# Kernel tuning notes

Measured on AMD Instinct MI355X. Metric: run time of the kernel, lower is better.

Reference implementation:

```python
import jax, jax.numpy as jnp
import numpy as np

N, E, D_IN, D_HID, D_OUT = 50000, 800000, 128, 128, 64

def setup_inputs() -> dict:
    key = jax.random.key(0)
    ks = jax.random.split(key, 20)
    inp = {
        'x': jax.random.normal(ks[0], (N, D_IN), dtype=jnp.float32),
        'edge_index': jax.random.randint(ks[1], (2, E), 0, N, dtype=jnp.int64),
        'edge_attr': jax.random.normal(ks[2], (E, 16), dtype=jnp.float32),
        'edge_weight': jax.random.uniform(ks[3], (E,), dtype=jnp.float32),
    }
    dims = [(D_IN, D_HID), (D_HID, D_HID), (D_HID, D_OUT)]
    for i, (di, do) in enumerate(dims):
        s = 1.0 / np.sqrt(di)
        inp[f'Wl{i}'] = jax.random.uniform(ks[4 + 5 * i], (di, do), minval=-s, maxval=s, dtype=jnp.float32)
        inp[f'bl{i}'] = jnp.zeros((do,), dtype=jnp.float32)
        inp[f'Wr{i}'] = jax.random.uniform(ks[5 + 5 * i], (di, do), minval=-s, maxval=s, dtype=jnp.float32)
        inp[f'Ws{i}'] = jax.random.uniform(ks[6 + 5 * i], (di, do), minval=-s, maxval=s, dtype=jnp.float32)
        inp[f'bs{i}'] = jnp.zeros((do,), dtype=jnp.float32)
    return inp


def _sage(x, src, dst, Wl, bl, Wr):
    # mean aggregation of source features at target nodes (PyG SAGEConv)
    msg = x[src]                                               # [E, d] gather
    ssum = jax.ops.segment_sum(msg, dst, num_segments=N)        # [N, d]
    cnt = jax.ops.segment_sum(jnp.ones((src.shape[0],), x.dtype), dst, num_segments=N)
    agg = ssum / jnp.maximum(cnt, 1.0)[:, None]
    return agg @ Wl + bl + x @ Wr                               # lin_l(agg) + lin_r(x)


def reference(x, edge_index, edge_attr, edge_weight,
              Wl0, bl0, Wr0, Ws0, bs0,
              Wl1, bl1, Wr1, Ws1, bs1,
              Wl2, bl2, Wr2, Ws2, bs2):
    src, dst = edge_index[0], edge_index[1]
    h = jax.nn.relu(_sage(x, src, dst, Wl0, bl0, Wr0) + x @ Ws0 + bs0)
    h = jax.nn.relu(_sage(h, src, dst, Wl1, bl1, Wr1) + h @ Ws1 + bs1)
    out = _sage(h, src, dst, Wl2, bl2, Wr2) + h @ Ws2 + bs2
    return out
```

## Files before the change

### kernel.cpp

```cpp
#include <hip/hip_runtime.h>
#include <hip/hip_bf16.h>


#define LB __launch_bounds__

typedef __attribute__((ext_vector_type(8))) short short8;
typedef __attribute__((ext_vector_type(4))) float f32x4;

__device__ __forceinline__ unsigned short bf16_rne(float f) {
  unsigned u = __builtin_bit_cast(unsigned, f);
  unsigned r = u + 0x7fffu + ((u >> 16) & 1u);
  return (unsigned short)(r >> 16);
}
__device__ __forceinline__ float bf16_to_f(unsigned short us) {
  return __builtin_bit_cast(float, (unsigned)us << 16);
}
__device__ __forceinline__ float bits_to_f(unsigned u) {
  return __builtin_bit_cast(float, u);
}

__device__ __forceinline__ void async16(const void* g, void* l) {
  __builtin_amdgcn_global_load_lds((const __attribute__((address_space(1))) unsigned*)g,
                                   (__attribute__((address_space(3))) unsigned*)l, 16, 0, 0);
}

#define BCAP 8192
#define P1_CHUNK 4096

__device__ __forceinline__ void p1_body(int bid, const int* __restrict__ src,
                                        const int* __restrict__ dst, int* __restrict__ bcnt,
                                        int2* __restrict__ pairs, int E) {
  __shared__ int cnt[256];
  __shared__ int base[256];
  const int tid = threadIdx.x;
  cnt[tid] = 0;
  __syncthreads();
  const int e0 = bid * P1_CHUNK;
  int myb[16], myr[16], mys[16], myd[16];
#pragma unroll
  for (int i = 0; i < 16; ++i) {
    int e = e0 + i * 256 + tid;
    myb[i] = -1;
    if (e < E) {
      int s = src[e], d = dst[e];
      int b = d >> 8;
      myb[i] = b;
      mys[i] = s;
      myd[i] = d;
      myr[i] = atomicAdd(&cnt[b], 1);
    }
  }
  __syncthreads();
  base[tid] = (cnt[tid] > 0) ? atomicAdd(&bcnt[tid], cnt[tid]) : 0;
  __syncthreads();
#pragma unroll
  for (int i = 0; i < 16; ++i) {
    int b = myb[i];
    if (b >= 0) {
      int p = base[b] + myr[i];
      if (p < BCAP) pairs[(size_t)b * BCAP + p] = make_int2(mys[i], myd[i]);
    }
  }
}

__device__ __forceinline__ void p234_body(int b, const int2* __restrict__ pairs,
                                          const int* __restrict__ bcnt, int* __restrict__ gcounter,
                                          int* __restrict__ row_start, int* __restrict__ deg_arr,
                                          float* __restrict__ scale, int* __restrict__ srcs, int N) {
  __shared__ int h[256];
  __shared__ int sc[256];
  __shared__ int cur[256];
  __shared__ int shared_bb;
  const int tid = threadIdx.x;
  h[tid] = 0;
  __syncthreads();
  int m = bcnt[b];
  if (m > BCAP) m = BCAP;
  for (int i = tid; i < m; i += 256) {
    atomicAdd(&h[pairs[(size_t)b * BCAP + i].y & 255], 1);
  }
  __syncthreads();
  const int deg = h[tid];
  sc[tid] = deg;
  __syncthreads();
  for (int off = 1; off < 256; off <<= 1) {
    int add = (tid >= off) ? sc[tid - off] : 0;
    __syncthreads();
    sc[tid] += add;
    __syncthreads();
  }
  if (tid == 0) shared_bb = atomicAdd(gcounter, sc[255]);
  __syncthreads();
  const int abs_off = shared_bb + sc[tid] - deg;
  const int node = b * 256 + tid;
  if (node < N) {
    row_start[node] = abs_off;
    deg_arr[node] = deg;
    scale[node] = 1.0f / (float)(deg > 1 ? deg : 1);
  }
  cur[tid] = abs_off;
  __syncthreads();
  for (int i = tid; i < m; i += 256) {
    int2 pr = pairs[(size_t)b * BCAP + i];
    int p = atomicAdd(&cur[pr.y & 255], 1);
    srcs[p] = pr.x;
  }
}

__device__ __forceinline__ void wpack_body(int wb, const float* __restrict__ Wl0,
                                           const float* __restrict__ Wr0,
                                           const float* __restrict__ Ws0,
                                           const float* __restrict__ bl0,
                                           const float* __restrict__ bs0,
                                           const float* __restrict__ Wl1,
                                           const float* __restrict__ Wr1,
                                           const float* __restrict__ Ws1,
                                           const float* __restrict__ bl1,
                                           const float* __restrict__ bs1,
                                           const float* __restrict__ Wl2,
                                           const float* __restrict__ Wr2,
                                           const float* __restrict__ Ws2,
                                           const float* __restrict__ bl2,
                                           const float* __restrict__ bs2, ushort* __restrict__ Bh0,
                                           ushort* __restrict__ Bo0, float* __restrict__ bb0,
                                           ushort* __restrict__ Bh1, ushort* __restrict__ Bo1,
                                           float* __restrict__ bb1, ushort* __restrict__ Bh2,
                                           ushort* __restrict__ Bo2, float* __restrict__ bb2) {
  const int layer = wb >> 7;
  const int xb = wb & 127;
  const float *Wl, *Wr, *Ws, *bl, *bs;
  ushort *Bh, *Bo;
  float* bb;
  int M;
  if (layer == 0) {
    Wl = Wl0; Wr = Wr0; Ws = Ws0; bl = bl0; bs = bs0; Bh = Bh0; Bo = Bo0; bb = bb0; M = 256;
  } else if (layer == 1) {
    Wl = Wl1; Wr = Wr1; Ws = Ws1; bl = bl1; bs = bs1; Bh = Bh1; Bo = Bo1; bb = bb1; M = 256;
  } else {
    Wl = Wl2; Wr = Wr2; Ws = Ws2; bl = bl2; bs = bs2; Bh = Bh2; Bo = Bo2; bb = bb2; M = 128;
  }
  const int DO = M / 2;
  int idx = xb * 256 + (int)threadIdx.x;
  if (idx < 128 * M) {
    int k = idx / M, c = idx - k * M;
    float v = (c < DO) ? Wl[k * DO + c] : (Wr[k * DO + (c - DO)] + Ws[k * DO + (c - DO)]);
    unsigned short h = bf16_rne(v);
    unsigned short l = bf16_rne(v - bf16_to_f(h));
    int d = ((k >> 3) * M + c) * 8 + (k & 7);
    Bh[d] = h;
    Bo[d] = l;
  }
  if (idx < DO) bb[idx] = bl[idx] + bs[idx];
}

__device__ __forceinline__ void split8v(f32x4 f0, f32x4 f1, short8& h, short8& l) {
  float f[8] = {f0[0], f0[1], f0[2], f0[3], f1[0], f1[1], f1[2], f1[3]};
#pragma unroll
  for (int j = 0; j < 8; ++j) {
    unsigned u = __builtin_bit_cast(unsigned, f[j]);
    h[j] = (short)(u >> 16);
    l[j] = (short)bf16_rne(f[j] - bits_to_f(u & 0xffff0000u));
  }
}

template <int M>
__device__ __forceinline__ void gemm_compute(int bx, const char* smem,
                                             const ushort* __restrict__ Bhi,
                                             const ushort* __restrict__ Blo,
                                             ushort* __restrict__ Yb, float* __restrict__ Z,
                                             int n) {
  constexpr int DO = M / 2;
  constexpr int NWC = (M >= 256) ? 4 : 2;
  constexpr int NWR = 4 / NWC;
  constexpr int BROWS = 32 * NWR;
  const int tid = threadIdx.x;
  const int w = tid >> 6, l = tid & 63;
  const int q = l >> 4, m16 = l & 15;
  const int rowBase = bx * BROWS + (w / NWC) * 32;
  const int colBase = (w % NWC) * 64;

  f32x4 acc[2][4] = {};
  const int rl0 = (w / NWC) * 32 + m16;

#pragma unroll
  for (int s = 0; s < 4; ++s) {
    short8 ah[2], al[2], bh[4], bo[4];
    const int kb = s * 4 + q;
#pragma unroll
    for (int i = 0; i < 2; ++i) {
      int rl = rl0 + i * 16;
      int g0 = (2 * kb) ^ m16;
      int g1 = (2 * kb + 1) ^ m16;
      f32x4 fa = *(const f32x4*)(smem + (size_t)rl * 512 + g0 * 16);
      f32x4 fb = *(const f32x4*)(smem + (size_t)rl * 512 + g1 * 16);
      split8v(fa, fb, ah[i], al[i]);
    }
#pragma unroll
    for (int j = 0; j < 4; ++j) {
      size_t off = ((size_t)kb * M + colBase + j * 16 + m16) * 8;
      bh[j] = *(const short8*)(Bhi + off);
      bo[j] = *(const short8*)(Blo + off);
    }
#pragma unroll
    for (int i = 0; i < 2; ++i)
#pragma unroll
      for (int j = 0; j < 4; ++j) {
        acc[i][j] = __builtin_amdgcn_mfma_f32_16x16x32_bf16(ah[i], bh[j], acc[i][j], 0, 0, 0);
        acc[i][j] = __builtin_amdgcn_mfma_f32_16x16x32_bf16(ah[i], bo[j], acc[i][j], 0, 0, 0);
        acc[i][j] = __builtin_amdgcn_mfma_f32_16x16x32_bf16(al[i], bh[j], acc[i][j], 0, 0, 0);
      }
  }

#pragma unroll
  for (int i = 0; i < 2; ++i) {
    int rb = rowBase + i * 16 + q * 4;
#pragma unroll
    for (int j = 0; j < 4; ++j) {
      int c = colBase + j * 16 + m16;
#pragma unroll
      for (int r = 0; r < 4; ++r) {
        int row = rb + r;
        if (row < n) {
          float v = acc[i][j][r];
          if (c < DO)
            Yb[(size_t)row * DO + c] = bf16_rne(v);
          else
            Z[(size_t)row * DO + (c - DO)] = v;
        }
      }
    }
  }
}

__device__ __forceinline__ void gemm0_body(int bx, const float* __restrict__ x,
                                           const ushort* __restrict__ Bh,
                                           const ushort* __restrict__ Bo, ushort* __restrict__ Yb,
                                           float* __restrict__ Z, int n, char* smem) {
  const int tid = threadIdx.x;
  const int wbase = tid & ~63;
#pragma unroll
  for (int r = 0; r < 4; ++r) {
    int ell = r * 256 + tid;
    int row = ell >> 5, gl = ell & 31;
    int grow = bx * 32 + row;
    if (grow >= n) grow = n - 1;
    int gs = gl ^ (row & 15);
    async16(x + (size_t)grow * 128 + gs * 4, smem + (size_t)(r * 256 + wbase) * 16);
  }
  __syncthreads();
  gemm_compute<256>(bx, smem, Bh, Bo, Yb, Z, n);
}

__device__ __forceinline__ void acc8(float* a, uint4 u) {
  a[0] += bits_to_f(u.x << 16);
  a[1] += bits_to_f(u.x & 0xffff0000u);
  a[2] += bits_to_f(u.y << 16);
  a[3] += bits_to_f(u.y & 0xffff0000u);
  a[4] += bits_to_f(u.z << 16);
  a[5] += bits_to_f(u.z & 0xffff0000u);
  a[6] += bits_to_f(u.w << 16);
  a[7] += bits_to_f(u.w & 0xffff0000u);
}

template <int M>
__global__ LB(256, (M >= 256 ? 5 : 4)) void fused_agg_gemm(
    const ushort* __restrict__ Y, const float* __restrict__ Zprev,
    const int* __restrict__ row_start, const int* __restrict__ deg_arr,
    const int* __restrict__ srcs, const float* __restrict__ scale,
    const float* __restrict__ bsum, const ushort* __restrict__ Bhi,
    const ushort* __restrict__ Blo, ushort* __restrict__ Yb, float* __restrict__ Zf, int n) {
  constexpr int BROWS = (M >= 256) ? 32 : 64;
  __shared__ __align__(16) char smem[BROWS * 512];
  const int tid = threadIdx.x;
  const int w = tid >> 6;
  const int lane = tid & 63;
  const int qt = lane >> 4;
  const int li = lane & 15;
  const int blockRow0 = blockIdx.x * BROWS;
  const uint4* Y4 = (const uint4*)Y;

#pragma unroll 1
  for (int t = 0; t < BROWS / 4; ++t) {
    const int r = t * 4 + w;
    const int node = blockRow0 + r;
    const bool live = node < n;
    float a[8] = {0.f, 0.f, 0.f, 0.f, 0.f, 0.f, 0.f, 0.f};
    float4 z0, z1, b0, b1;
    float sc = 0.f;
    if (live) {
      const int e0 = row_start[node];
      const int cnt = deg_arr[node];
      const int c1 = cnt < 64 ? cnt : 64;
      int idx = (lane < c1) ? srcs[e0 + lane] : 0;
      if (qt == 0) {
        sc = scale[node];
        z0 = ((const float4*)Zprev)[(size_t)node * 32 + 2 * li];
        z1 = ((const float4*)Zprev)[(size_t)node * 32 + 2 * li + 1];
        b0 = ((const float4*)bsum)[2 * li];
        b1 = ((const float4*)bsum)[2 * li + 1];
      }
      int j = 0;
      for (; j + 16 <= c1; j += 16) {
        int s0 = __shfl(idx, j + qt);
        int s1 = __shfl(idx, j + 4 + qt);
        int s2 = __shfl(idx, j + 8 + qt);
        int s3 = __shfl(idx, j + 12 + qt);
        uint4 u0 = Y4[(size_t)s0 * 16 + li];
        uint4 u1 = Y4[(size_t)s1 * 16 + li];
        uint4 u2 = Y4[(size_t)s2 * 16 + li];
        uint4 u3 = Y4[(size_t)s3 * 16 + li];
        acc8(a, u0);
        acc8(a, u1);
        acc8(a, u2);
        acc8(a, u3);
      }
      for (; j + 4 <= c1; j += 4) {
        int s = __shfl(idx, j + qt);
        uint4 u = Y4[(size_t)s * 16 + li];
        acc8(a, u);
      }
      {
        int rem = c1 - j;
        if (rem > 0) {
          int s = __shfl(idx, j + (qt < rem ? qt : 0));
          if (qt < rem) {
            uint4 u = Y4[(size_t)s * 16 + li];
            acc8(a, u);
          }
        }
      }
      if (cnt > 64) {
        int e = 64;
        for (; e + 4 <= cnt; e += 4) {
          int s = srcs[e0 + e + qt];
          uint4 u = Y4[(size_t)s * 16 + li];
          acc8(a, u);
        }
        int rem = cnt - e;
        if (qt < rem) {
          int s = srcs[e0 + e + qt];
          uint4 u = Y4[(size_t)s * 16 + li];
          acc8(a, u);
        }
      }
    }
#pragma unroll
    for (int k = 0; k < 8; ++k) {
      a[k] += __shfl(a[k], lane ^ 16);
      a[k] += __shfl(a[k], lane ^ 32);
    }
    float4 o0 = make_float4(0.f, 0.f, 0.f, 0.f);
    float4 o1 = make_float4(0.f, 0.f, 0.f, 0.f);
    if (live && qt == 0) {
      o0.x = fmaxf(z0.x + sc * a[0] + b0.x, 0.f);
      o0.y = fmaxf(z0.y + sc * a[1] + b0.y, 0.f);
      o0.z = fmaxf(z0.z + sc * a[2] + b0.z, 0.f);
      o0.w = fmaxf(z0.w + sc * a[3] + b0.w, 0.f);
      o1.x = fmaxf(z1.x + sc * a[4] + b1.x, 0.f);
      o1.y = fmaxf(z1.y + sc * a[5] + b1.y, 0.f);
      o1.z = fmaxf(z1.z + sc * a[6] + b1.z, 0.f);
      o1.w = fmaxf(z1.w + sc * a[7] + b1.w, 0.f);
    }
    if (qt == 0) {
      *(float4*)(smem + (size_t)r * 512 + (size_t)(((2 * li) ^ (r & 15)) * 16)) = o0;
      *(float4*)(smem + (size_t)r * 512 + (size_t)(((2 * li + 1) ^ (r & 15)) * 16)) = o1;
    }
  }
  __syncthreads();
  gemm_compute<M>(blockIdx.x, smem, Bhi, Blo, Yb, Zf, n);
}

__global__ LB(256) void fused_wpack_p1(const int* __restrict__ src, const int* __restrict__ dst,
                                       int* __restrict__ bcnt, int2* __restrict__ pairs, int E,
                                       int NP1, const float* Wl0, const float* Wr0, const float* Ws0,
                                       const float* bl0, const float* bs0, const float* Wl1,
                                       const float* Wr1, const float* Ws1, const float* bl1,
                                       const float* bs1, const float* Wl2, const float* Wr2,
                                       const float* Ws2, const float* bl2, const float* bs2,
                                       ushort* Bh0, ushort* Bo0, float* bb0, ushort* Bh1,
                                       ushort* Bo1, float* bb1, ushort* Bh2, ushort* Bo2,
                                       float* bb2) {
  if ((int)blockIdx.x < NP1) {
    p1_body(blockIdx.x, src, dst, bcnt, pairs, E);
  } else {
    wpack_body(blockIdx.x - NP1, Wl0, Wr0, Ws0, bl0, bs0, Wl1, Wr1, Ws1, bl1, bs1, Wl2, Wr2, Ws2,
               bl2, bs2, Bh0, Bo0, bb0, Bh1, Bo1, bb1, Bh2, Bo2, bb2);
  }
}

__global__ LB(256, 5) void fused_p234_gemm0(const int2* __restrict__ pairs,
                                            const int* __restrict__ bcnt, int* __restrict__ gcounter,
                                            int* __restrict__ row_start, int* __restrict__ deg_arr,
                                            float* __restrict__ scale, int* __restrict__ srcs, int N,
                                            const float* __restrict__ x,
                                            const ushort* __restrict__ Bh0,
                                            const ushort* __restrict__ Bo0, ushort* __restrict__ Yb,
                                            float* __restrict__ Zf, int NB) {
  __shared__ __align__(16) char smem[32 * 512];
  if ((int)blockIdx.x < NB) {
    p234_body(blockIdx.x, pairs, bcnt, gcounter, row_start, deg_arr, scale, srcs, N);
  } else {
    gemm0_body(blockIdx.x - NB, x, Bh0, Bo0, Yb, Zf, N, smem);
  }
}

__global__ LB(256) void agg64_kernel(const ushort* __restrict__ Y, const float* __restrict__ Z,
                                     const int* __restrict__ row_start,
                                     const int* __restrict__ deg_arr, const int* __restrict__ srcs,
                                     const float* __restrict__ scale, const float* __restrict__ bsum,
                                     float* __restrict__ out, int n) {
  int node = blockIdx.x * 4 + (threadIdx.x >> 6);
  if (node >= n) return;
  const int lane = threadIdx.x & 63;
  const int li = lane & 15;
  const int qt = lane >> 4;
  const int e0 = row_start[node];
  const int cnt = deg_arr[node];
  const int end = e0 + cnt;
  const int c1 = cnt < 64 ? cnt : 64;
  int idx = (lane < c1) ? srcs[e0 + lane] : 0;
  const uint2* Yu = (const uint2*)Y;
  float a0 = 0.f, a1 = 0.f, a2 = 0.f, a3 = 0.f;

  int j = 0;
  for (; j + 16 <= c1; j += 16) {
    int s0 = __shfl(idx, j + qt);
    int s1 = __shfl(idx, j + 4 + qt);
    int s2 = __shfl(idx, j + 8 + qt);
    int s3 = __shfl(idx, j + 12 + qt);
    uint2 u0 = Yu[(size_t)s0 * 16 + li];
    uint2 u1 = Yu[(size_t)s1 * 16 + li];
    uint2 u2 = Yu[(size_t)s2 * 16 + li];
    uint2 u3 = Yu[(size_t)s3 * 16 + li];
    a0 += bits_to_f(u0.x << 16) + bits_to_f(u1.x << 16) + bits_to_f(u2.x << 16) +
          bits_to_f(u3.x << 16);
    a1 += bits_to_f(u0.x & 0xffff0000u) + bits_to_f(u1.x & 0xffff0000u) +
          bits_to_f(u2.x & 0xffff0000u) + bits_to_f(u3.x & 0xffff0000u);
    a2 += bits_to_f(u0.y << 16) + bits_to_f(u1.y << 16) + bits_to_f(u2.y << 16) +
          bits_to_f(u3.y << 16);
    a3 += bits_to_f(u0.y & 0xffff0000u) + bits_to_f(u1.y & 0xffff0000u) +
          bits_to_f(u2.y & 0xffff0000u) + bits_to_f(u3.y & 0xffff0000u);
  }
  for (; j + 4 <= c1; j += 4) {
    int s = __shfl(idx, j + qt);
    uint2 u = Yu[(size_t)s * 16 + li];
    a0 += bits_to_f(u.x << 16);
    a1 += bits_to_f(u.x & 0xffff0000u);
    a2 += bits_to_f(u.y << 16);
    a3 += bits_to_f(u.y & 0xffff0000u);
  }
  {
    int rem = c1 - j;
    if (rem > 0) {
      int s = __shfl(idx, j + (qt < rem ? qt : 0));
      if (qt < rem) {
        uint2 u = Yu[(size_t)s * 16 + li];
        a0 += bits_to_f(u.x << 16);
        a1 += bits_to_f(u.x & 0xffff0000u);
        a2 += bits_to_f(u.y << 16);
        a3 += bits_to_f(u.y & 0xffff0000u);
      }
    }
  }
  if (cnt > 64) {
    int e = e0 + 64;
    for (; e + 4 <= end; e += 4) {
      int s = srcs[e + qt];
      uint2 u = Yu[(size_t)s * 16 + li];
      a0 += bits_to_f(u.x << 16);
      a1 += bits_to_f(u.x & 0xffff0000u);
      a2 += bits_to_f(u.y << 16);
      a3 += bits_to_f(u.y & 0xffff0000u);
    }
    int rem = end - e;
    if (qt < rem) {
      int s = srcs[e + qt];
      uint2 u = Yu[(size_t)s * 16 + li];
      a0 += bits_to_f(u.x << 16);
      a1 += bits_to_f(u.x & 0xffff0000u);
      a2 += bits_to_f(u.y << 16);
      a3 += bits_to_f(u.y & 0xffff0000u);
    }
  }
  a0 += __shfl(a0, lane ^ 16);
  a1 += __shfl(a1, lane ^ 16);
  a2 += __shfl(a2, lane ^ 16);
  a3 += __shfl(a3, lane ^ 16);
  a0 += __shfl(a0, lane ^ 32);
  a1 += __shfl(a1, lane ^ 32);
  a2 += __shfl(a2, lane ^ 32);
  a3 += __shfl(a3, lane ^ 32);

  if (qt == 0) {
    float sc = scale[node];
    float4 z = ((const float4*)Z)[(size_t)node * 16 + li];
    float4 b = ((const float4*)bsum)[li];
    float4 o;
    o.x = z.x + sc * a0 + b.x;
    o.y = z.y + sc * a1 + b.y;
    o.z = z.z + sc * a2 + b.z;
    o.w = z.w + sc * a3 + b.w;
    ((float4*)out)[(size_t)node * 16 + li] = o;
  }
}

extern "C" void kernel_launch(void* const* d_in, const int* in_sizes, int n_in,
                              void* d_out, int out_size, void* d_ws, size_t ws_size,
                              hipStream_t stream) {
  const float* x = (const float*)d_in[0];
  const int* ei = (const int*)d_in[1];
  const int N = in_sizes[0] / 128;
  const int E = in_sizes[3];
  const int* src = ei;
  const int* dst = ei + E;
  const float* Wl[3] = {(const float*)d_in[4], (const float*)d_in[9], (const float*)d_in[14]};
  const float* bl[3] = {(const float*)d_in[5], (const float*)d_in[10], (const float*)d_in[15]};
  const float* Wr[3] = {(const float*)d_in[6], (const float*)d_in[11], (const float*)d_in[16]};
  const float* Ws[3] = {(const float*)d_in[7], (const float*)d_in[12], (const float*)d_in[17]};
  const float* bs[3] = {(const float*)d_in[8], (const float*)d_in[13], (const float*)d_in[18]};

  const int NB = (N + 255) >> 8;
  const int NP1 = (E + P1_CHUNK - 1) / P1_CHUNK;

  size_t off = 0;
  auto carve = [&](size_t bytes) -> char* {
    char* p = (char*)d_ws + off;
    off += (bytes + 255) & ~(size_t)255;
    return p;
  };
  int* row_start = (int*)carve((size_t)N * 4);
  int* deg_arr = (int*)carve((size_t)N * 4);
  int* bcnt = (int*)carve((size_t)NB * 4);
  int* gcounter = (int*)carve(256);
  float* scale = (float*)carve((size_t)N * 4);
  int* srcs = (int*)carve((size_t)E * 4);
  int2* pairs = (int2*)carve((size_t)NB * BCAP * 8);
  ushort* Yb0 = (ushort*)carve((size_t)N * 128 * 2);
  float* Zf0 = (float*)carve((size_t)N * 128 * 4);
  ushort* Yb1 = (ushort*)carve((size_t)N * 128 * 2);
  float* Zf1 = (float*)carve((size_t)N * 128 * 4);
  ushort* Bh[3];
  ushort* Bo[3];
  float* bsum[3];
  for (int i = 0; i < 3; ++i) {
    Bh[i] = (ushort*)carve(128 * 256 * 2);
    Bo[i] = (ushort*)carve(128 * 256 * 2);
    bsum[i] = (float*)carve(128 * 4);
  }
  (void)ws_size;
  (void)n_in;
  (void)out_size;

  size_t bcnt_pad = ((size_t)NB * 4 + 255) & ~(size_t)255;
  hipMemsetAsync(bcnt, 0, bcnt_pad + 4, stream);

  fused_wpack_p1<<<NP1 + 384, 256, 0, stream>>>(
      src, dst, bcnt, pairs, E, NP1, Wl[0], Wr[0], Ws[0], bl[0], bs[0], Wl[1], Wr[1], Ws[1], bl[1],
      bs[1], Wl[2], Wr[2], Ws[2], bl[2], bs[2], Bh[0], Bo[0], bsum[0], Bh[1], Bo[1], bsum[1], Bh[2],
      Bo[2], bsum[2]);

  int g32 = (N + 31) / 32;
  int g64 = (N + 63) / 64;
  int gAgg = (N + 3) / 4;

  fused_p234_gemm0<<<NB + g32, 256, 0, stream>>>(pairs, bcnt, gcounter, row_start, deg_arr, scale,
                                                 srcs, N, x, Bh[0], Bo[0], Yb0, Zf0, NB);
  fused_agg_gemm<256><<<g32, 256, 0, stream>>>(Yb0, Zf0, row_start, deg_arr, srcs, scale, bsum[0],
                                               Bh[1], Bo[1], Yb1, Zf1, N);
  fused_agg_gemm<128><<<g64, 256, 0, stream>>>(Yb1, Zf1, row_start, deg_arr, srcs, scale, bsum[1],
                                               Bh[2], Bo[2], Yb0, Zf0, N);
  agg64_kernel<<<gAgg, 256, 0, stream>>>(Yb0, Zf0, row_start, deg_arr, srcs, scale, bsum[2],
                                         (float*)d_out, N);
}
```

Baseline: 305.2 us.

## Map one node per quarter-wave in aggregation kernels with 8-deep gather batching

Aggregation in the fused agg+GEMM kernels and the final agg64 kernel now assigns each 16-lane quarter-wave its own node instead of one node per wavefront. Each lane gathers 8 neighbor rows in flight before accumulating, and the cross-quarter shuffle reduction is removed. The intent is to cut per-node overhead (index broadcast, reduction, idle lanes on low-degree nodes) and to expose more memory-level parallelism for the random gathers. The cost is divergence within a wave when the four nodes have different degrees, since the loop runs to the wave-wide max degree with predicated loads. Register pressure is also higher from the 8-wide buffers.

```diff
diff --git a/kernel.cpp b/kernel.cpp
--- a/kernel.cpp
+++ b/kernel.cpp
@@ -263,12 +263,16 @@
 }
 
 template <int M>
-__global__ LB(256, (M >= 256 ? 5 : 4)) void fused_agg_gemm(
-    const ushort* __restrict__ Y, const float* __restrict__ Zprev,
-    const int* __restrict__ row_start, const int* __restrict__ deg_arr,
-    const int* __restrict__ srcs, const float* __restrict__ scale,
-    const float* __restrict__ bsum, const ushort* __restrict__ Bhi,
-    const ushort* __restrict__ Blo, ushort* __restrict__ Yb, float* __restrict__ Zf, int n) {
+__global__ LB(256, 4) void fused_agg_gemm(const ushort* __restrict__ Y,
+                                          const float* __restrict__ Zprev,
+                                          const int* __restrict__ row_start,
+                                          const int* __restrict__ deg_arr,
+                                          const int* __restrict__ srcs,
+                                          const float* __restrict__ scale,
+                                          const float* __restrict__ bsum,
+                                          const ushort* __restrict__ Bhi,
+                                          const ushort* __restrict__ Blo, ushort* __restrict__ Yb,
+                                          float* __restrict__ Zf, int n) {
   constexpr int BROWS = (M >= 256) ? 32 : 64;
   __shared__ __align__(16) char smem[BROWS * 512];
   const int tid = threadIdx.x;
@@ -280,91 +284,54 @@
   const uint4* Y4 = (const uint4*)Y;
 
 #pragma unroll 1
-  for (int t = 0; t < BROWS / 4; ++t) {
-    const int r = t * 4 + w;
+  for (int t = 0; t < BROWS / 16; ++t) {
+    const int r = t * 16 + w * 4 + qt;
     const int node = blockRow0 + r;
     const bool live = node < n;
+    const int cn = live ? node : n - 1;
+    const int e0q = row_start[cn];
+    const int cntq = live ? deg_arr[cn] : 0;
+    const float sc = scale[cn];
+    float4 z0 = ((const float4*)Zprev)[(size_t)cn * 32 + 2 * li];
+    float4 z1 = ((const float4*)Zprev)[(size_t)cn * 32 + 2 * li + 1];
+    float4 b0 = ((const float4*)bsum)[2 * li];
+    float4 b1 = ((const float4*)bsum)[2 * li + 1];
     float a[8] = {0.f, 0.f, 0.f, 0.f, 0.f, 0.f, 0.f, 0.f};
-    float4 z0, z1, b0, b1;
-    float sc = 0.f;
-    if (live) {
-      const int e0 = row_start[node];
-      const int cnt = deg_arr[node];
-      const int c1 = cnt < 64 ? cnt : 64;
-      int idx = (lane < c1) ? srcs[e0 + lane] : 0;
-      if (qt == 0) {
-        sc = scale[node];
-        z0 = ((const float4*)Zprev)[(size_t)node * 32 + 2 * li];
-        z1 = ((const float4*)Zprev)[(size_t)node * 32 + 2 * li + 1];
-        b0 = ((const float4*)bsum)[2 * li];
-        b1 = ((const float4*)bsum)[2 * li + 1];
+
+    int cm = cntq;
+    cm = max(cm, __shfl_xor(cm, 16));
+    cm = max(cm, __shfl_xor(cm, 32));
+
+    for (int base = 0; base < cm; base += 16) {
+      int idx = (base + li < cntq) ? srcs[e0q + base + li] : 0;
+      int lim = cm - base;
+      if (lim > 16) lim = 16;
+      for (int jj = 0; jj < lim; jj += 8) {
+        int s[8];
+#pragma unroll
+        for (int k = 0; k < 8; ++k) s[k] = __shfl(idx, (qt << 4) + jj + k);
+        uint4 u[8];
+#pragma unroll
+        for (int k = 0; k < 8; ++k) {
+          uint4 v = make_uint4(0u, 0u, 0u, 0u);
+          if (base + jj + k < cntq) v = Y4[(size_t)s[k] * 16 + li];
+          u[k] = v;
+        }
+#pragma unroll
+        for (int k = 0; k < 8; ++k) acc8(a, u[k]);
       }
-      int j = 0;
-      for (; j + 16 <= c1; j += 16) {
-        int s0 = __shfl(idx, j + qt);
-        int s1 = __shfl(idx, j + 4 + qt);
-        int s2 = __shfl(idx, j + 8 + qt);
-        int s3 = __shfl(idx, j + 12 + qt);
-        uint4 u0 = Y4[(size_t)s0 * 16 + li];
-        uint4 u1 = Y4[(size_t)s1 * 16 + li];
-        uint4 u2 = Y4[(size_t)s2 * 16 + li];
-        uint4 u3 = Y4[(size_t)s3 * 16 + li];
-        acc8(a, u0);
-        acc8(a, u1);
-        acc8(a, u2);
-        acc8(a, u3);
-      }
-      for (; j + 4 <= c1; j += 4) {
-        int s = __shfl(idx, j + qt);
-        uint4 u = Y4[(size_t)s * 16 + li];
-        acc8(a, u);
-      }
-      {
-        int rem = c1 - j;
-        if (rem > 0) {
-          int s = __shfl(idx, j + (qt < rem ? qt : 0));
-          if (qt < rem) {
-            uint4 u = Y4[(size_t)s * 16 + li];
-            acc8(a, u);
-          }
-        }
-      }
-      if (cnt > 64) {
-        int e = 64;
-        for (; e + 4 <= cnt; e += 4) {
-          int s = srcs[e0 + e + qt];
-          uint4 u = Y4[(size_t)s * 16 + li];
-          acc8(a, u);
-        }
-        int rem = cnt - e;
-        if (qt < rem) {
-          int s = srcs[e0 + e + qt];
-          uint4 u = Y4[(size_t)s * 16 + li];
-          acc8(a, u);
-        }
-      }
-    }
-#pragma unroll
-    for (int k = 0; k < 8; ++k) {
-      a[k] += __shfl(a[k], lane ^ 16);
-      a[k] += __shfl(a[k], lane ^ 32);
-    }
-    float4 o0 = make_float4(0.f, 0.f, 0.f, 0.f);
-    float4 o1 = make_float4(0.f, 0.f, 0.f, 0.f);
-    if (live && qt == 0) {
-      o0.x = fmaxf(z0.x + sc * a[0] + b0.x, 0.f);
-      o0.y = fmaxf(z0.y + sc * a[1] + b0.y, 0.f);
-      o0.z = fmaxf(z0.z + sc * a[2] + b0.z, 0.f);
-      o0.w = fmaxf(z0.w + sc * a[3] + b0.w, 0.f);
-      o1.x = fmaxf(z1.x + sc * a[4] + b1.x, 0.f);
-      o1.y = fmaxf(z1.y + sc * a[5] + b1.y, 0.f);
-      o1.z = fmaxf(z1.z + sc * a[6] + b1.z, 0.f);
-      o1.w = fmaxf(z1.w + sc * a[7] + b1.w, 0.f);
-    }
-    if (qt == 0) {
-      *(float4*)(smem + (size_t)r * 512 + (size_t)(((2 * li) ^ (r & 15)) * 16)) = o0;
-      *(float4*)(smem + (size_t)r * 512 + (size_t)(((2 * li + 1) ^ (r & 15)) * 16)) = o1;
-    }
+    }
+    float4 o0, o1;
+    o0.x = fmaxf(z0.x + sc * a[0] + b0.x, 0.f);
+    o0.y = fmaxf(z0.y + sc * a[1] + b0.y, 0.f);
+    o0.z = fmaxf(z0.z + sc * a[2] + b0.z, 0.f);
+    o0.w = fmaxf(z0.w + sc * a[3] + b0.w, 0.f);
+    o1.x = fmaxf(z1.x + sc * a[4] + b1.x, 0.f);
+    o1.y = fmaxf(z1.y + sc * a[5] + b1.y, 0.f);
+    o1.z = fmaxf(z1.z + sc * a[6] + b1.z, 0.f);
+    o1.w = fmaxf(z1.w + sc * a[7] + b1.w, 0.f);
+    *(float4*)(smem + (size_t)r * 512 + (size_t)(((2 * li) ^ (r & 15)) * 16)) = o0;
+    *(float4*)(smem + (size_t)r * 512 + (size_t)(((2 * li + 1) ^ (r & 15)) * 16)) = o1;
   }
   __syncthreads();
   gemm_compute<M>(blockIdx.x, smem, Bhi, Blo, Yb, Zf, n);
@@ -404,97 +371,56 @@
   }
 }
 
-__global__ LB(256) void agg64_kernel(const ushort* __restrict__ Y, const float* __restrict__ Z,
-                                     const int* __restrict__ row_start,
-                                     const int* __restrict__ deg_arr, const int* __restrict__ srcs,
-                                     const float* __restrict__ scale, const float* __restrict__ bsum,
-                                     float* __restrict__ out, int n) {
-  int node = blockIdx.x * 4 + (threadIdx.x >> 6);
-  if (node >= n) return;
-  const int lane = threadIdx.x & 63;
+__global__ LB(256, 4) void agg64_kernel(const ushort* __restrict__ Y, const float* __restrict__ Z,
+                                        const int* __restrict__ row_start,
+                                        const int* __restrict__ deg_arr, const int* __restrict__ srcs,
+                                        const float* __restrict__ scale,
+                                        const float* __restrict__ bsum, float* __restrict__ out,
+                                        int n) {
+  const int tid = threadIdx.x;
+  const int lane = tid & 63;
+  const int qt = lane >> 4;
   const int li = lane & 15;
-  const int qt = lane >> 4;
-  const int e0 = row_start[node];
-  const int cnt = deg_arr[node];
-  const int end = e0 + cnt;
-  const int c1 = cnt < 64 ? cnt : 64;
-  int idx = (lane < c1) ? srcs[e0 + lane] : 0;
+  const int node = blockIdx.x * 16 + (tid >> 6) * 4 + qt;
+  const bool live = node < n;
+  const int cn = live ? node : n - 1;
+  const int e0q = row_start[cn];
+  const int cntq = live ? deg_arr[cn] : 0;
   const uint2* Yu = (const uint2*)Y;
   float a0 = 0.f, a1 = 0.f, a2 = 0.f, a3 = 0.f;
-
-  int j = 0;
-  for (; j + 16 <= c1; j += 16) {
-    int s0 = __shfl(idx, j + qt);
-    int s1 = __shfl(idx, j + 4 + qt);
-    int s2 = __shfl(idx, j + 8 + qt);
-    int s3 = __shfl(idx, j + 12 + qt);
-    uint2 u0 = Yu[(size_t)s0 * 16 + li];
-    uint2 u1 = Yu[(size_t)s1 * 16 + li];
-    uint2 u2 = Yu[(size_t)s2 * 16 + li];
-    uint2 u3 = Yu[(size_t)s3 * 16 + li];
-    a0 += bits_to_f(u0.x << 16) + bits_to_f(u1.x << 16) + bits_to_f(u2.x << 16) +
-          bits_to_f(u3.x << 16);
-    a1 += bits_to_f(u0.x & 0xffff0000u) + bits_to_f(u1.x & 0xffff0000u) +
-          bits_to_f(u2.x & 0xffff0000u) + bits_to_f(u3.x & 0xffff0000u);
-    a2 += bits_to_f(u0.y << 16) + bits_to_f(u1.y << 16) + bits_to_f(u2.y << 16) +
-          bits_to_f(u3.y << 16);
-    a3 += bits_to_f(u0.y & 0xffff0000u) + bits_to_f(u1.y & 0xffff0000u) +
-          bits_to_f(u2.y & 0xffff0000u) + bits_to_f(u3.y & 0xffff0000u);
-  }
-  for (; j + 4 <= c1; j += 4) {
-    int s = __shfl(idx, j + qt);
-    uint2 u = Yu[(size_t)s * 16 + li];
-    a0 += bits_to_f(u.x << 16);
-    a1 += bits_to_f(u.x & 0xffff0000u);
-    a2 += bits_to_f(u.y << 16);
-    a3 += bits_to_f(u.y & 0xffff0000u);
-  }
-  {
-    int rem = c1 - j;
-    if (rem > 0) {
-      int s = __shfl(idx, j + (qt < rem ? qt : 0));
-      if (qt < rem) {
-        uint2 u = Yu[(size_t)s * 16 + li];
-        a0 += bits_to_f(u.x << 16);
-        a1 += bits_to_f(u.x & 0xffff0000u);
-        a2 += bits_to_f(u.y << 16);
-        a3 += bits_to_f(u.y & 0xffff0000u);
+  const float sc = scale[cn];
+  float4 z = ((const float4*)Z)[(size_t)cn * 16 + li];
+  float4 b = ((const float4*)bsum)[li];
+
+  int cm = cntq;
+  cm = max(cm, __shfl_xor(cm, 16));
+  cm = max(cm, __shfl_xor(cm, 32));
+
+  for (int base = 0; base < cm; base += 16) {
+    int idx = (base + li < cntq) ? srcs[e0q + base + li] : 0;
+    int lim = cm - base;
+    if (lim > 16) lim = 16;
+    for (int jj = 0; jj < lim; jj += 8) {
+      int s[8];
+#pragma unroll
+      for (int k = 0; k < 8; ++k) s[k] = __shfl(idx, (qt << 4) + jj + k);
+      uint2 u[8];
+#pragma unroll
+      for (int k = 0; k < 8; ++k) {
+        uint2 v = make_uint2(0u, 0u);
+        if (base + jj + k < cntq) v = Yu[(size_t)s[k] * 16 + li];
+        u[k] = v;
       }
-    }
-  }
-  if (cnt > 64) {
-    int e = e0 + 64;
-    for (; e + 4 <= end; e += 4) {
-      int s = srcs[e + qt];
-      uint2 u = Yu[(size_t)s * 16 + li];
-      a0 += bits_to_f(u.x << 16);
-      a1 += bits_to_f(u.x & 0xffff0000u);
-      a2 += bits_to_f(u.y << 16);
-      a3 += bits_to_f(u.y & 0xffff0000u);
-    }
-    int rem = end - e;
-    if (qt < rem) {
-      int s = srcs[e + qt];
-      uint2 u = Yu[(size_t)s * 16 + li];
-      a0 += bits_to_f(u.x << 16);
-      a1 += bits_to_f(u.x & 0xffff0000u);
-      a2 += bits_to_f(u.y << 16);
-      a3 += bits_to_f(u.y & 0xffff0000u);
-    }
-  }
-  a0 += __shfl(a0, lane ^ 16);
-  a1 += __shfl(a1, lane ^ 16);
-  a2 += __shfl(a2, lane ^ 16);
-  a3 += __shfl(a3, lane ^ 16);
-  a0 += __shfl(a0, lane ^ 32);
-  a1 += __shfl(a1, lane ^ 32);
-  a2 += __shfl(a2, lane ^ 32);
-  a3 += __shfl(a3, lane ^ 32);
-
-  if (qt == 0) {
-    float sc = scale[node];
-    float4 z = ((const float4*)Z)[(size_t)node * 16 + li];
-    float4 b = ((const float4*)bsum)[li];
+#pragma unroll
+      for (int k = 0; k < 8; ++k) {
+        a0 += bits_to_f(u[k].x << 16);
+        a1 += bits_to_f(u[k].x & 0xffff0000u);
+        a2 += bits_to_f(u[k].y << 16);
+        a3 += bits_to_f(u[k].y & 0xffff0000u);
+      }
+    }
+  }
+  if (live) {
     float4 o;
     o.x = z.x + sc * a0 + b.x;
     o.y = z.y + sc * a1 + b.y;
@@ -561,7 +487,7 @@
 
   int g32 = (N + 31) / 32;
   int g64 = (N + 63) / 64;
-  int gAgg = (N + 3) / 4;
+  int gAgg = (N + 15) / 16;
 
   fused_p234_gemm0<<<NB + g32, 256, 0, stream>>>(pairs, bcnt, gcounter, row_start, deg_arr, scale,
                                                  srcs, N, x, Bh[0], Bo[0], Yb0, Zf0, NB);
```

Result: faster. 277.3 us (-9.2%).
